# Kernel optimization log

Hardware: AMD Instinct MI355X
Metric: run time of the kernel (lower is better)

Reference implementation:

```python
import jax, jax.numpy as jnp
import numpy as np

B, T, C, H = 4, 2048, 1024, 16
D = C // H
SCALE = D ** -0.5


def setup_inputs() -> dict:
    key = jax.random.key(0)
    ks = jax.random.split(key, 5)
    x = jax.random.normal(ks[0], (B, T, C), dtype=jnp.float32)
    key_padding_mask = jnp.zeros((B, T), dtype=bool)  # True = masked key
    W_qkv = jax.random.normal(ks[1], (C, 3 * C), dtype=jnp.float32) * (C ** -0.5)
    b_qkv = jax.random.normal(ks[2], (3 * C,), dtype=jnp.float32) * 0.02
    W_proj = jax.random.normal(ks[3], (C, C), dtype=jnp.float32) * (C ** -0.5)
    b_proj = jax.random.normal(ks[4], (C,), dtype=jnp.float32) * 0.02
    return {"x": x, "key_padding_mask": key_padding_mask, "W_qkv": W_qkv,
            "b_qkv": b_qkv, "W_proj": W_proj, "b_proj": b_proj}


def reference(x, key_padding_mask, W_qkv, b_qkv, W_proj, b_proj):
    Bx, Tx, Cx = x.shape
    qkv = x @ W_qkv + b_qkv                      # [B,T,3C]
    qkv = qkv.reshape(Bx, Tx, 3, H, D)
    q = jnp.transpose(qkv[:, :, 0], (0, 2, 1, 3))  # [B,H,T,D]
    k = jnp.transpose(qkv[:, :, 1], (0, 2, 1, 3))
    v = jnp.transpose(qkv[:, :, 2], (0, 2, 1, 3))
    attn = jnp.einsum('bhqd,bhkd->bhqk', q, k) * SCALE  # [B,H,T,T]
    causal = jnp.triu(jnp.ones((Tx, Tx), dtype=bool), k=1)  # True = masked
    neg_inf = jnp.finfo(attn.dtype).min
    attn = jnp.where(causal[None, None, :, :], neg_inf, attn)
    attn = jnp.where(key_padding_mask[:, None, None, :], neg_inf, attn)
    attn = jax.nn.softmax(attn, axis=-1)
    out = jnp.einsum('bhqk,bhkd->bhqd', attn, v)  # [B,H,T,D]
    out = jnp.transpose(out, (0, 2, 1, 3)).reshape(Bx, Tx, Cx)
    return out @ W_proj + b_proj
```

## Files before the change

kernel.cpp:

```cpp
#include <hip/hip_runtime.h>


typedef __bf16 bf16;
typedef __bf16 bf16x4 __attribute__((ext_vector_type(4)));
typedef __bf16 bf16x8 __attribute__((ext_vector_type(8)));
typedef float f32x4 __attribute__((ext_vector_type(4)));

#define MFMA(a, b, c) __builtin_amdgcn_mfma_f32_16x16x32_bf16((a), (b), (c), 0, 0, 0)

typedef const __attribute__((address_space(1))) void* gas_ptr;
typedef __attribute__((address_space(3))) void* las_ptr;

__device__ __forceinline__ void gload_lds16(const bf16* g, bf16* lds) {
  __builtin_amdgcn_global_load_lds((gas_ptr)g, (las_ptr)lds, 16, 0, 0);
}

__global__ __launch_bounds__(256) void k_cvt(const float* __restrict__ src,
                                             bf16* __restrict__ dst, int n4) {
  int i = blockIdx.x * 256 + threadIdx.x;
  if (i >= n4) return;
  float4 v = ((const float4*)src)[i];
  bf16x4 o = { (bf16)v.x, (bf16)v.y, (bf16)v.z, (bf16)v.w };
  ((bf16x4*)dst)[i] = o;
}

__global__ __launch_bounds__(256) void k_transpose(const float* __restrict__ src,
                                                   bf16* __restrict__ dst,
                                                   int R, int C) {
  __shared__ float tile[32][33];
  int c0 = blockIdx.x * 32, r0 = blockIdx.y * 32;
  int x = threadIdx.x & 31, y = threadIdx.x >> 5;
#pragma unroll
  for (int i = 0; i < 4; ++i)
    tile[y + i * 8][x] = src[(size_t)(r0 + y + i * 8) * C + (c0 + x)];
  __syncthreads();
#pragma unroll
  for (int i = 0; i < 4; ++i)
    dst[(size_t)(c0 + y + i * 8) * R + (r0 + x)] = (bf16)tile[x][y + i * 8];
}

__global__ void k_maskflags(const unsigned char* __restrict__ kpm,
                            int* __restrict__ flags) {
  int i = threadIdx.x;
  const uint4* p = (const uint4*)(kpm + i * 128);
  unsigned acc = 0;
#pragma unroll
  for (int j = 0; j < 8; ++j) { uint4 v = p[j]; acc |= v.x | v.y | v.z | v.w; }
  flags[i] = (acc != 0) ? 1 : 0;
}

template <int EPI>
__global__ __launch_bounds__(256, 2)
void k_gemm_bt(const bf16* __restrict__ A, const bf16* __restrict__ Bt,
               const float* __restrict__ bias, float* __restrict__ fout,
               bf16* __restrict__ qp, bf16* __restrict__ kp,
               bf16* __restrict__ vtp, int M, int N, int K) {
  __shared__ bf16 Ab[2][128 * 32];
  __shared__ bf16 Bb[2][128 * 32];
  const int tid = threadIdx.x;
  const int wave = tid >> 6, lane = tid & 63;
  const int m0 = blockIdx.x * 128, n0 = blockIdx.y * 128;
  const int wr = wave >> 1, wc = wave & 1;
  const int lrow = lane & 15, kb = (lane >> 4) * 8;
  f32x4 acc[4][4] = {};
  const int nkt = K >> 5;

  auto stage = [&](int buf, int kt) {
#pragma unroll
    for (int i = 0; i < 2; ++i) {
      int c = i * 4 + wave;
      const bf16* ga = A + (size_t)(m0 + c * 16 + (lane >> 2)) * K + kt * 32 + (lane & 3) * 8;
      gload_lds16(ga, &Ab[buf][c * 512]);
      const bf16* gb = Bt + (size_t)(n0 + c * 16 + (lane >> 2)) * K + kt * 32 + (lane & 3) * 8;
      gload_lds16(gb, &Bb[buf][c * 512]);
    }
  };

  stage(0, 0);
  asm volatile("s_waitcnt vmcnt(0)" ::: "memory");
  __syncthreads();
  int cur = 0;
  for (int kt = 0; kt < nkt; ++kt) {
    if (kt + 1 < nkt) stage(cur ^ 1, kt + 1);
    bf16x8 af[4], bfr[4];
#pragma unroll
    for (int m = 0; m < 4; ++m)
      af[m] = *(const bf16x8*)&Ab[cur][(wr * 64 + m * 16 + lrow) * 32 + kb];
#pragma unroll
    for (int n = 0; n < 4; ++n)
      bfr[n] = *(const bf16x8*)&Bb[cur][(wc * 64 + n * 16 + lrow) * 32 + kb];
#pragma unroll
    for (int m = 0; m < 4; ++m)
#pragma unroll
      for (int n = 0; n < 4; ++n)
        acc[m][n] = MFMA(af[m], bfr[n], acc[m][n]);
    asm volatile("s_waitcnt vmcnt(0)" ::: "memory");
    __syncthreads();
    cur ^= 1;
  }

#pragma unroll
  for (int m = 0; m < 4; ++m) {
#pragma unroll
    for (int n = 0; n < 4; ++n) {
      const int col = n0 + wc * 64 + n * 16 + lrow;
      const int row0 = m0 + wr * 64 + m * 16 + (lane >> 4) * 4;
      const float bv = bias[col];
      if (EPI == 0) {
        const int which = col >> 10;
        const int h = (col >> 6) & 15, d = col & 63;
        const int b = row0 >> 11, t0 = row0 & 2047;
        const int bh = b * 16 + h;
        if (which == 2) {
          bf16x4 pk;
#pragma unroll
          for (int j = 0; j < 4; ++j) pk[j] = (bf16)(acc[m][n][j] + bv);
          *(bf16x4*)&vtp[((size_t)bh * 64 + d) * 2048 + t0] = pk;
        } else {
          bf16* dstp = (which == 0) ? qp : kp;
          const float sc = (which == 0) ? 0.18033688011112042f : 1.0f;
#pragma unroll
          for (int j = 0; j < 4; ++j)
            dstp[((size_t)bh * 2048 + (t0 + j)) * 64 + d] = (bf16)((acc[m][n][j] + bv) * sc);
        }
      } else {
#pragma unroll
        for (int j = 0; j < 4; ++j)
          fout[(size_t)(row0 + j) * N + col] = acc[m][n][j] + bv;
      }
    }
  }
}

__global__ __launch_bounds__(256, 2)
void k_flash(const bf16* __restrict__ Q, const bf16* __restrict__ Kg,
             const bf16* __restrict__ Vt, const unsigned char* __restrict__ kpm,
             const int* __restrict__ tflags, bf16* __restrict__ O) {
  const int bh = blockIdx.y;
  const int b = bh >> 4, h = bh & 15;
  const int tid = threadIdx.x, wave = tid >> 6, lane = tid & 63;
  const int lrow = lane & 15, g = lane >> 4;

  __shared__ bf16 Kt[128 * 64];
  __shared__ bf16 Vts[64 * 128];
  __shared__ bf16 PT[4][2][2048];

  const bf16* Kbh = Kg + (size_t)bh * 2048 * 64;
  const bf16* Vbh = Vt + (size_t)bh * 64 * 2048;

  const int k_src_col = (((lane & 7) ^ (lane >> 3)) << 3);
  const int k_row_in_chunk = lane >> 3;

  const int ptb2 = g * 256 + lrow * 8;

  for (int pass = 0; pass < 2; ++pass) {
    const int qt = pass ? (15 - (int)blockIdx.x) : (int)blockIdx.x;

    const bf16* Qbase = Q + ((size_t)bh * 2048 + qt * 128 + wave * 32) * 64;
    bf16x8 qf[2][2];
#pragma unroll
    for (int m = 0; m < 2; ++m)
#pragma unroll
      for (int ks = 0; ks < 2; ++ks)
        qf[m][ks] = *(const bf16x8*)&Qbase[(m * 16 + lrow) * 64 + ks * 32 + g * 8];

    f32x4 oacc[2][4] = {};
    float rm[2][4], rl[2][4];
#pragma unroll
    for (int m = 0; m < 2; ++m)
#pragma unroll
      for (int j = 0; j < 4; ++j) { rm[m][j] = -1e30f; rl[m][j] = 0.f; }

    for (int kvt = 0; kvt <= qt; ++kvt) {
#pragma unroll
      for (int i = 0; i < 4; ++i) {
        int c = i * 4 + wave;
        gload_lds16(Kbh + (size_t)(kvt * 128 + c * 8 + k_row_in_chunk) * 64 + k_src_col,
                    &Kt[c * 512]);
      }
#pragma unroll
      for (int i = 0; i < 4; ++i) {
        int c = i * 4 + wave;
        int vs = (((lane & 15) ^ (((c & 1) << 2) | g)) << 3);
        gload_lds16(Vbh + (size_t)(c * 4 + g) * 2048 + kvt * 128 + vs, &Vts[c * 512]);
      }
      asm volatile("s_waitcnt vmcnt(0)" ::: "memory");
      __syncthreads();

      f32x4 s[2][8];
#pragma unroll
      for (int n = 0; n < 8; ++n) {
        const int row = n * 16 + lrow;
        bf16x8 kf0 = *(const bf16x8*)&Kt[row * 64 + ((g ^ (lrow & 7)) << 3)];
        bf16x8 kf1 = *(const bf16x8*)&Kt[row * 64 + (((4 + g) ^ (lrow & 7)) << 3)];
#pragma unroll
        for (int m = 0; m < 2; ++m) {
          f32x4 t = {};
          t = MFMA(qf[m][0], kf0, t);
          t = MFMA(qf[m][1], kf1, t);
          s[m][n] = t;
        }
      }

      if (tflags[b * 16 + kvt]) {
#pragma unroll
        for (int n = 0; n < 8; ++n) {
          const int col = kvt * 128 + n * 16 + lrow;
          if (kpm[b * 2048 + col]) {
#pragma unroll
            for (int m = 0; m < 2; ++m)
#pragma unroll
              for (int j = 0; j < 4; ++j) s[m][n][j] = -1e30f;
          }
        }
      }
      if (kvt == qt) {
#pragma unroll
        for (int n = 0; n < 8; ++n) {
          const int col = n * 16 + lrow;
#pragma unroll
          for (int m = 0; m < 2; ++m)
#pragma unroll
            for (int j = 0; j < 4; ++j) {
              const int row = wave * 32 + m * 16 + g * 4 + j;
              if (col > row) s[m][n][j] = -1e30f;
            }
        }
      }

      float tmax[2][4];
#pragma unroll
      for (int m = 0; m < 2; ++m)
#pragma unroll
        for (int j = 0; j < 4; ++j) {
          float v = s[m][0][j];
#pragma unroll
          for (int n = 1; n < 8; ++n) v = fmaxf(v, s[m][n][j]);
          tmax[m][j] = v;
        }
#pragma unroll
      for (int off = 1; off < 16; off <<= 1)
#pragma unroll
        for (int m = 0; m < 2; ++m)
#pragma unroll
          for (int j = 0; j < 4; ++j)
            tmax[m][j] = fmaxf(tmax[m][j], __shfl_xor(tmax[m][j], off, 64));

      bool need = false;
#pragma unroll
      for (int m = 0; m < 2; ++m)
#pragma unroll
        for (int j = 0; j < 4; ++j) need |= (tmax[m][j] > rm[m][j] + 8.f);
      if (__any(need)) {
#pragma unroll
        for (int m = 0; m < 2; ++m)
#pragma unroll
          for (int j = 0; j < 4; ++j) {
            const float mn = fmaxf(rm[m][j], tmax[m][j]);
            const float f = exp2f(rm[m][j] - mn);
            rm[m][j] = mn;
            rl[m][j] *= f;
#pragma unroll
            for (int nt = 0; nt < 4; ++nt) oacc[m][nt][j] *= f;
          }
      }

      float rs[2][4] = {};
#pragma unroll
      for (int m = 0; m < 2; ++m)
#pragma unroll
        for (int n = 0; n < 8; ++n) {
          bf16x4 pk;
#pragma unroll
          for (int j = 0; j < 4; ++j) {
            const float p = exp2f(s[m][n][j] - rm[m][j]);
            rs[m][j] += p;
            pk[j] = (bf16)p;
          }
          const int woff = (n * 16 + lrow) * 32 + g * 8;
          *(bf16x4*)((char*)&PT[wave][m][0] + woff) = pk;
        }
#pragma unroll
      for (int off = 1; off < 16; off <<= 1)
#pragma unroll
        for (int m = 0; m < 2; ++m)
#pragma unroll
          for (int j = 0; j < 4; ++j) rs[m][j] += __shfl_xor(rs[m][j], off, 64);
#pragma unroll
      for (int m = 0; m < 2; ++m)
#pragma unroll
        for (int j = 0; j < 4; ++j) rl[m][j] += rs[m][j];

      asm volatile("s_waitcnt lgkmcnt(0)" ::: "memory");
      __builtin_amdgcn_sched_barrier(0);
#pragma unroll
      for (int ks = 0; ks < 4; ++ks) {
        bf16x4 plo[2], phi[2];
#pragma unroll
        for (int m = 0; m < 2; ++m) {
          las_ptr pa_ = (las_ptr)((char*)&PT[wave][m][0] + ptb2);
          asm volatile("ds_read_b64_tr_b16 %0, %1 offset:%2"
                       : "=v"(plo[m]) : "v"(pa_), "i"(ks * 1024));
          asm volatile("ds_read_b64_tr_b16 %0, %1 offset:%2"
                       : "=v"(phi[m]) : "v"(pa_), "i"(ks * 1024 + 128));
        }
        bf16x8 vf[4];
#pragma unroll
        for (int nt = 0; nt < 4; ++nt) {
          const int d = nt * 16 + lrow;
          vf[nt] = *(const bf16x8*)((const char*)Vts + d * 256 +
                                    (((ks * 4 + g) ^ (lrow & 7)) << 4));
        }
        asm volatile("s_waitcnt lgkmcnt(0)" ::: "memory");
        __builtin_amdgcn_sched_barrier(0);
#pragma unroll
        for (int nt = 0; nt < 4; ++nt)
#pragma unroll
          for (int m = 0; m < 2; ++m) {
            bf16x8 pa = __builtin_shufflevector(plo[m], phi[m], 0, 1, 2, 3, 4, 5, 6, 7);
            oacc[m][nt] = MFMA(pa, vf[nt], oacc[m][nt]);
          }
      }
      __syncthreads();
    }

#pragma unroll
    for (int m = 0; m < 2; ++m)
#pragma unroll
      for (int nt = 0; nt < 4; ++nt)
#pragma unroll
        for (int j = 0; j < 4; ++j) {
          const int t = qt * 128 + wave * 32 + m * 16 + g * 4 + j;
          const int c = h * 64 + nt * 16 + lrow;
          O[((size_t)b * 2048 + t) * 1024 + c] = (bf16)(oacc[m][nt][j] / rl[m][j]);
        }
  }
}

extern "C" void kernel_launch(void* const* d_in, const int* in_sizes, int n_in,
                              void* d_out, int out_size, void* d_ws, size_t ws_size,
                              hipStream_t stream) {
  const float* x = (const float*)d_in[0];
  const unsigned char* kpm = (const unsigned char*)d_in[1];
  const float* Wqkv = (const float*)d_in[2];
  const float* bqkv = (const float*)d_in[3];
  const float* Wproj = (const float*)d_in[4];
  const float* bproj = (const float*)d_in[5];
  float* out = (float*)d_out;
  char* ws = (char*)d_ws;

  bf16* xb     = (bf16*)(ws + 0);
  bf16* WqkvT  = (bf16*)(ws + 16777216);
  bf16* WprojT = (bf16*)(ws + 23068672);
  bf16* Qb     = (bf16*)(ws + 25165824);
  bf16* Kb     = (bf16*)(ws + 41943040);
  bf16* Vtb    = (bf16*)(ws + 58720256);
  bf16* AOb    = (bf16*)(ws + 75497472);
  int*  tflags = (int*)(ws + 0);

  k_cvt<<<8192, 256, 0, stream>>>(x, xb, 2097152);
  k_transpose<<<dim3(96, 32), 256, 0, stream>>>(Wqkv, WqkvT, 1024, 3072);
  k_transpose<<<dim3(32, 32), 256, 0, stream>>>(Wproj, WprojT, 1024, 1024);
  k_gemm_bt<0><<<dim3(64, 24), 256, 0, stream>>>(xb, WqkvT, bqkv, nullptr, Qb, Kb,
                                                 Vtb, 8192, 3072, 1024);
  k_maskflags<<<1, 64, 0, stream>>>(kpm, tflags);
  k_flash<<<dim3(8, 64), 256, 0, stream>>>(Qb, Kb, Vtb, kpm, tflags, AOb);
  k_gemm_bt<1><<<dim3(64, 8), 256, 0, stream>>>(AOb, WprojT, bproj, out, nullptr,
                                                nullptr, nullptr, 8192, 1024, 1024);
}
```

Baseline: 210.3 us.

## Double-buffer K tiles in flash attention and defer row-sum reduction

The flash kernel now double-buffers K in LDS, prefetching the next KV tile's K while computing QK^T on the current one. V is issued at loop start and waited on only before the PV MFMAs. The per-tile cross-lane row-sum shuffle reduction is moved to a single reduction after the KV loop, and the max is computed as a tree. The grid is also transposed so consecutive blocks share the same query tile across heads. This adds LDS use (an extra 16KB K buffer), which may affect the two-blocks-per-CU occupancy, and adds an extra barrier per iteration.

```diff
diff --git a/kernel.cpp b/kernel.cpp
--- a/kernel.cpp
+++ b/kernel.cpp
@@ -136,12 +136,13 @@
 void k_flash(const bf16* __restrict__ Q, const bf16* __restrict__ Kg,
              const bf16* __restrict__ Vt, const unsigned char* __restrict__ kpm,
              const int* __restrict__ tflags, bf16* __restrict__ O) {
-  const int bh = blockIdx.y;
+  const int bh = blockIdx.x;
   const int b = bh >> 4, h = bh & 15;
+  const int w = blockIdx.y;
   const int tid = threadIdx.x, wave = tid >> 6, lane = tid & 63;
   const int lrow = lane & 15, g = lane >> 4;
 
-  __shared__ bf16 Kt[128 * 64];
+  __shared__ bf16 Kt[2][128 * 64];
   __shared__ bf16 Vts[64 * 128];
   __shared__ bf16 PT[4][2][2048];
 
@@ -153,8 +154,26 @@
 
   const int ptb2 = g * 256 + lrow * 8;
 
+  auto stageK = [&](int buf, int kvt) {
+#pragma unroll
+    for (int i = 0; i < 4; ++i) {
+      int c = i * 4 + wave;
+      gload_lds16(Kbh + (size_t)(kvt * 128 + c * 8 + k_row_in_chunk) * 64 + k_src_col,
+                  &Kt[buf][c * 512]);
+    }
+  };
+  auto stageV = [&](int kvt) {
+#pragma unroll
+    for (int i = 0; i < 4; ++i) {
+      int c = i * 4 + wave;
+      int vs = (((lane & 15) ^ (((c & 1) << 2) | g)) << 3);
+      gload_lds16(Vbh + (size_t)(c * 4 + g) * 2048 + kvt * 128 + vs, &Vts[c * 512]);
+    }
+  };
+
+  int cur = 0;
   for (int pass = 0; pass < 2; ++pass) {
-    const int qt = pass ? (15 - (int)blockIdx.x) : (int)blockIdx.x;
+    const int qt = pass ? (15 - w) : w;
 
     const bf16* Qbase = Q + ((size_t)bh * 2048 + qt * 128 + wave * 32) * 64;
     bf16x8 qf[2][2];
@@ -171,28 +190,22 @@
 #pragma unroll
       for (int j = 0; j < 4; ++j) { rm[m][j] = -1e30f; rl[m][j] = 0.f; }
 
+    stageK(cur, 0);
+    asm volatile("s_waitcnt vmcnt(0)" ::: "memory");
+    __builtin_amdgcn_s_barrier();
+    __builtin_amdgcn_sched_barrier(0);
+
     for (int kvt = 0; kvt <= qt; ++kvt) {
-#pragma unroll
-      for (int i = 0; i < 4; ++i) {
-        int c = i * 4 + wave;
-        gload_lds16(Kbh + (size_t)(kvt * 128 + c * 8 + k_row_in_chunk) * 64 + k_src_col,
-                    &Kt[c * 512]);
-      }
-#pragma unroll
-      for (int i = 0; i < 4; ++i) {
-        int c = i * 4 + wave;
-        int vs = (((lane & 15) ^ (((c & 1) << 2) | g)) << 3);
-        gload_lds16(Vbh + (size_t)(c * 4 + g) * 2048 + kvt * 128 + vs, &Vts[c * 512]);
-      }
-      asm volatile("s_waitcnt vmcnt(0)" ::: "memory");
-      __syncthreads();
+      const bool pref = (kvt < qt);
+      stageV(kvt);
+      if (pref) stageK(cur ^ 1, kvt + 1);
 
       f32x4 s[2][8];
 #pragma unroll
       for (int n = 0; n < 8; ++n) {
         const int row = n * 16 + lrow;
-        bf16x8 kf0 = *(const bf16x8*)&Kt[row * 64 + ((g ^ (lrow & 7)) << 3)];
-        bf16x8 kf1 = *(const bf16x8*)&Kt[row * 64 + (((4 + g) ^ (lrow & 7)) << 3)];
+        bf16x8 kf0 = *(const bf16x8*)&Kt[cur][row * 64 + ((g ^ (lrow & 7)) << 3)];
+        bf16x8 kf1 = *(const bf16x8*)&Kt[cur][row * 64 + (((4 + g) ^ (lrow & 7)) << 3)];
 #pragma unroll
         for (int m = 0; m < 2; ++m) {
           f32x4 t = {};
@@ -233,10 +246,11 @@
       for (int m = 0; m < 2; ++m)
 #pragma unroll
         for (int j = 0; j < 4; ++j) {
-          float v = s[m][0][j];
-#pragma unroll
-          for (int n = 1; n < 8; ++n) v = fmaxf(v, s[m][n][j]);
-          tmax[m][j] = v;
+          float v01 = fmaxf(s[m][0][j], s[m][1][j]);
+          float v23 = fmaxf(s[m][2][j], s[m][3][j]);
+          float v45 = fmaxf(s[m][4][j], s[m][5][j]);
+          float v67 = fmaxf(s[m][6][j], s[m][7][j]);
+          tmax[m][j] = fmaxf(fmaxf(v01, v23), fmaxf(v45, v67));
         }
 #pragma unroll
       for (int off = 1; off < 16; off <<= 1)
@@ -265,7 +279,6 @@
           }
       }
 
-      float rs[2][4] = {};
 #pragma unroll
       for (int m = 0; m < 2; ++m)
 #pragma unroll
@@ -274,25 +287,18 @@
 #pragma unroll
           for (int j = 0; j < 4; ++j) {
             const float p = exp2f(s[m][n][j] - rm[m][j]);
-            rs[m][j] += p;
+            rl[m][j] += p;
             pk[j] = (bf16)p;
           }
           const int woff = (n * 16 + lrow) * 32 + g * 8;
           *(bf16x4*)((char*)&PT[wave][m][0] + woff) = pk;
         }
-#pragma unroll
-      for (int off = 1; off < 16; off <<= 1)
-#pragma unroll
-        for (int m = 0; m < 2; ++m)
-#pragma unroll
-          for (int j = 0; j < 4; ++j) rs[m][j] += __shfl_xor(rs[m][j], off, 64);
-#pragma unroll
-      for (int m = 0; m < 2; ++m)
-#pragma unroll
-        for (int j = 0; j < 4; ++j) rl[m][j] += rs[m][j];
-
-      asm volatile("s_waitcnt lgkmcnt(0)" ::: "memory");
+
+      if (pref) asm volatile("s_waitcnt vmcnt(4)" ::: "memory");
+      else      asm volatile("s_waitcnt vmcnt(0)" ::: "memory");
+      __builtin_amdgcn_s_barrier();
       __builtin_amdgcn_sched_barrier(0);
+
 #pragma unroll
       for (int ks = 0; ks < 4; ++ks) {
         bf16x4 plo[2], phi[2];
@@ -321,8 +327,19 @@
             oacc[m][nt] = MFMA(pa, vf[nt], oacc[m][nt]);
           }
       }
-      __syncthreads();
-    }
+
+      asm volatile("s_waitcnt vmcnt(0)" ::: "memory");
+      __builtin_amdgcn_s_barrier();
+      __builtin_amdgcn_sched_barrier(0);
+      cur ^= 1;
+    }
+
+#pragma unroll
+    for (int off = 1; off < 16; off <<= 1)
+#pragma unroll
+      for (int m = 0; m < 2; ++m)
+#pragma unroll
+        for (int j = 0; j < 4; ++j) rl[m][j] += __shfl_xor(rl[m][j], off, 64);
 
 #pragma unroll
     for (int m = 0; m < 2; ++m)
@@ -364,7 +381,7 @@
   k_gemm_bt<0><<<dim3(64, 24), 256, 0, stream>>>(xb, WqkvT, bqkv, nullptr, Qb, Kb,
                                                  Vtb, 8192, 3072, 1024);
   k_maskflags<<<1, 64, 0, stream>>>(kpm, tflags);
-  k_flash<<<dim3(8, 64), 256, 0, stream>>>(Qb, Kb, Vtb, kpm, tflags, AOb);
+  k_flash<<<dim3(64, 8), 256, 0, stream>>>(Qb, Kb, Vtb, kpm, tflags, AOb);
   k_gemm_bt<1><<<dim3(64, 8), 256, 0, stream>>>(AOb, WprojT, bproj, out, nullptr,
                                                 nullptr, nullptr, 8192, 1024, 1024);
 }
```

Result: faster. 201.7 us (-4.1%).
